# Performance work log

Hardware: AMD Instinct MI355X
Metric: run time of the kernel (lower is better)

The kernel has to match this reference:

```python
import jax, jax.numpy as jnp
import numpy as np

MARGIN = 0.5
BETA = 0.0
K = 5

def setup_inputs() -> dict:
    key = jax.random.key(0)
    k1, k2 = jax.random.split(key)
    n, d, n_classes = 4096, 512, 512
    inputs = jax.random.normal(k1, (n, d), dtype=jnp.float32)
    # L2-normalize as is standard for similarity-based DML embeddings
    inputs = inputs / jnp.linalg.norm(inputs, axis=1, keepdims=True)
    targets = jax.random.randint(k2, (n,), 0, n_classes, dtype=jnp.int64)
    return {"inputs": inputs, "targets": targets}

def reference(inputs, targets):
    n = inputs.shape[0]
    sim = inputs @ inputs.T                      # [n, n] similarity matrix
    same = targets[:, None] == targets[None, :]  # [n, n] same-class mask
    eye = jnp.eye(n, dtype=bool)
    pos_mask = same & ~eye                       # positive pairs (off-diagonal)
    neg_mask = ~same                             # negative pairs
    # margin_loss (hinge on similarity): pos -> [margin + beta - s]_+, neg -> [margin + s - beta]_+
    pos_l = jnp.maximum(MARGIN + BETA - sim, 0.0)
    neg_l = jnp.maximum(MARGIN + sim - BETA, 0.0)
    valid = pos_mask | neg_mask
    pair_loss = jnp.where(pos_mask, pos_l, neg_l)  # per-pair loss where valid
    num_of_zeros = jnp.sum(valid & (pair_loss == 0.0))
    # top-(4K) over the multiset of all valid pair losses (== topk of concat(pos_loss, neg_loss))
    masked = jnp.where(valid, pair_loss, -jnp.inf).reshape(-1)
    top_loss, _ = jax.lax.top_k(masked, 4 * K)
    loss = jnp.mean(top_loss)
    mean_pos_sim = jnp.sum(jnp.where(pos_mask, sim, 0.0)) / jnp.sum(pos_mask)
    mean_neg_sim = jnp.sum(jnp.where(neg_mask, sim, 0.0)) / jnp.sum(neg_mask)
    # NOTE: the original swaps the names: it returns mean(pos_sim) as `mean_neg_sim` and vice versa.
    return (loss, num_of_zeros, mean_pos_sim, mean_neg_sim)
```

## Files before the change

### kernel.cpp

```cpp
#include <hip/hip_runtime.h>
#include <hip/hip_fp16.h>

constexpr int N = 4096;
constexpr int D = 512;
constexpr int NT = 32;
constexpr int NBLK = NT * (NT + 1) / 2;
constexpr float SENT = -1e30f;
constexpr unsigned TCV = 8386560u;

constexpr float T0 = 0.60f;
constexpr unsigned CCAP = 320;

typedef _Float16 f16x8 __attribute__((ext_vector_type(8)));
typedef float f32x4 __attribute__((ext_vector_type(4)));

__device__ __forceinline__ void load_lds16(const _Float16* g, _Float16* l) {
  __builtin_amdgcn_global_load_lds(
      (const __attribute__((address_space(1))) void*)g,
      (__attribute__((address_space(3))) void*)l, 16, 0, 0);
}

template <int M>
__device__ __forceinline__ void wave_sel10(float (&vals)[M], float (&out)[10]) {
  int lane = threadIdx.x & 63;
  float lm = vals[0];
#pragma unroll
  for (int k = 1; k < M; k++) lm = fmaxf(lm, vals[k]);
#pragma unroll
  for (int r = 0; r < 10; r++) {
    float wmx = lm;
#pragma unroll
    for (int ofs = 1; ofs < 64; ofs <<= 1)
      wmx = fmaxf(wmx, __shfl_xor(wmx, ofs));
    out[r] = wmx;
    unsigned long long b = __ballot(lm == wmx);
    int leader = __ffsll(b) - 1;
    if (lane == leader) {
      bool found = false;
#pragma unroll
      for (int k = 0; k < M; k++) {
        bool hit = !found && (vals[k] == wmx);
        vals[k] = hit ? SENT : vals[k];
        found = found || hit;
      }
      lm = vals[0];
#pragma unroll
      for (int k = 1; k < M; k++) lm = fmaxf(lm, vals[k]);
    }
  }
}

constexpr int BMAX_IDX = 3 * NBLK;
constexpr int TOP10G_IDX = 4 * NBLK;
constexpr int XH_OFF = 32768;

__global__ void prep_kernel(const float4* __restrict__ X4,
                            ushort4* __restrict__ Xh4) {
  int gid = blockIdx.x * 256 + threadIdx.x;
  float4 v = X4[gid];
  ushort4 o;
  o.x = __half_as_ushort(__float2half_rn(v.x));
  o.y = __half_as_ushort(__float2half_rn(v.y));
  o.z = __half_as_ushort(__float2half_rn(v.z));
  o.w = __half_as_ushort(__float2half_rn(v.w));
  Xh4[gid] = o;
}

__global__ __launch_bounds__(256, 3) void gemm_stats_kernel(
    const _Float16* __restrict__ Xh, const int* __restrict__ tgt,
    float* __restrict__ slots, float* __restrict__ top10g) {
  __shared__ _Float16 As[2][128 * 32];
  __shared__ _Float16 Bs[2][128 * 32];
  __shared__ int tA[128], tB[128];
  __shared__ float redf[2][4];
  __shared__ unsigned redu[4];
  __shared__ float redm[4];
  __shared__ unsigned redc[4];
  __shared__ float cbuf[CCAP];
  __shared__ unsigned ccnt;
  __shared__ unsigned scc;

  int tid = threadIdx.x;
  if (tid == 0) ccnt = 0u;

  int id = blockIdx.x, br = 0;
  while (id >= (NT - br)) { id -= (NT - br); br++; }
  int bc = br + id;

  if (tid < 128) tA[tid] = tgt[br * 128 + tid];
  else tB[tid - 128] = tgt[bc * 128 + (tid - 128)];

  int lane = tid & 63, wave = tid >> 6;
  int wm2 = (wave >> 1) << 6;
  int wn2 = (wave & 1) << 6;
  int lrow = lane & 15;
  int q4 = lane >> 4;
  int xk = (lrow >> 1) & 3;
  int quad4 = q4 * 4;

  int srow[2], scol[2], sdst[2];
#pragma unroll
  for (int i = 0; i < 2; i++) {
    int C = i * 256 + tid;
    int row = C >> 2, p = C & 3;
    srow[i] = row;
    scol[i] = (p ^ ((row >> 1) & 3)) * 8;
    sdst[i] = (i * 4 + wave) * 512;
  }
  const _Float16* Arow = Xh + (size_t)(br * 128) * D;
  const _Float16* Brow = Xh + (size_t)(bc * 128) * D;

#pragma unroll
  for (int i = 0; i < 2; i++) {
    load_lds16(Arow + srow[i] * D + scol[i], &As[0][sdst[i]]);
    load_lds16(Brow + srow[i] * D + scol[i], &Bs[0][sdst[i]]);
  }

  f32x4 acc[4][4] = {};
#pragma unroll
  for (int t = 0; t < 16; t++) {
    int cur = t & 1;
    __syncthreads();
    if (t < 15) {
      int k0 = (t + 1) * 32;
#pragma unroll
      for (int i = 0; i < 2; i++) {
        load_lds16(Arow + srow[i] * D + k0 + scol[i], &As[cur ^ 1][sdst[i]]);
        load_lds16(Brow + srow[i] * D + k0 + scol[i], &Bs[cur ^ 1][sdst[i]]);
      }
    }
    f16x8 af[4], bf[4];
#pragma unroll
    for (int mi = 0; mi < 4; mi++)
      af[mi] = *(const f16x8*)&As[cur][(wm2 + mi * 16 + lrow) * 32 +
                                       (q4 ^ xk) * 8];
#pragma unroll
    for (int ni = 0; ni < 4; ni++)
      bf[ni] = *(const f16x8*)&Bs[cur][(wn2 + ni * 16 + lrow) * 32 +
                                       (q4 ^ xk) * 8];
#pragma unroll
    for (int mi = 0; mi < 4; mi++)
#pragma unroll
      for (int ni = 0; ni < 4; ni++)
        acc[mi][ni] = __builtin_amdgcn_mfma_f32_16x16x32_f16(
            af[mi], bf[ni], acc[mi][ni], 0, 0, 0);
  }

  int tj[4];
#pragma unroll
  for (int ni = 0; ni < 4; ni++) tj[ni] = tB[wn2 + ni * 16 + lrow];
  int ib = br * 128 + wm2 + quad4;
  int jb = bc * 128 + wn2 + lrow;

  auto forEachLoss = [&](auto&& fn) {
#pragma unroll
    for (int mi = 0; mi < 4; mi++) {
#pragma unroll
      for (int r = 0; r < 4; r++) {
        int trow = tA[wm2 + mi * 16 + quad4 + r];
        int i = ib + mi * 16 + r;
#pragma unroll
        for (int ni = 0; ni < 4; ni++) {
          float s = acc[mi][ni][r];
          int j = jb + ni * 16;
          bool valid = j > i;
          bool pos = valid && (trow == tj[ni]);
          float loss = fmaxf(0.5f + (pos ? -s : s), 0.0f);
          fn(s, loss, valid, pos);
        }
      }
    }
  };

  float lsv = 0.f, lsp = 0.f, tmax = SENT;
  unsigned cz = 0, cc = 0;
  float b0 = 0.f, b1 = 0.f, b2 = 0.f, b3 = 0.f;
  forEachLoss([&](float s, float loss, bool valid, bool pos) {
    if (valid) {
      lsv += s;
      if (loss == 0.0f) cz += 0x10000u;
      tmax = fmaxf(tmax, loss);
      if (loss >= T0) {
        if (cc == 0) b0 = loss;
        else if (cc == 1) b1 = loss;
        else if (cc == 2) b2 = loss;
        else if (cc == 3) b3 = loss;
        else {
          unsigned op = atomicAdd(&ccnt, 1u);
          if (op < CCAP) cbuf[op] = loss;
        }
        cc++;
      }
    }
    if (pos) { lsp += s; cz += 1u; }
  });

  float lmax = tmax;
#pragma unroll
  for (int o = 32; o > 0; o >>= 1) {
    lsv += __shfl_down(lsv, o);
    lsp += __shfl_down(lsp, o);
    cz += __shfl_down(cz, o);
    lmax = fmaxf(lmax, __shfl_down(lmax, o));
  }
  if (lane == 0) {
    redf[0][wave] = lsv; redf[1][wave] = lsp;
    redu[wave] = cz; redm[wave] = lmax;
  }

  unsigned cnt4 = cc < 4u ? cc : 4u;
  unsigned inc = cnt4;
#pragma unroll
  for (int o = 1; o < 64; o <<= 1) {
    unsigned tt = __shfl_up(inc, o);
    if (lane >= o) inc += tt;
  }
  unsigned base = 0;
  if (lane == 63) base = atomicAdd(&ccnt, inc);
  base = __shfl(base, 63);
  unsigned p = base + inc - cnt4;
  if (cnt4 > 0u && p < CCAP) cbuf[p] = b0;
  if (cnt4 > 1u && p + 1 < CCAP) cbuf[p + 1] = b1;
  if (cnt4 > 2u && p + 2 < CCAP) cbuf[p + 2] = b2;
  if (cnt4 > 3u && p + 3 < CCAP) cbuf[p + 3] = b3;
  __syncthreads();

  if (tid == 192) {
    float a = redf[0][0] + redf[0][1] + redf[0][2] + redf[0][3];
    float b = redf[1][0] + redf[1][1] + redf[1][2] + redf[1][3];
    unsigned c = redu[0] + redu[1] + redu[2] + redu[3];
    float bm = fmaxf(fmaxf(redm[0], redm[1]), fmaxf(redm[2], redm[3]));
    slots[blockIdx.x] = a;
    slots[NBLK + blockIdx.x] = b;
    ((unsigned*)slots)[2 * NBLK + blockIdx.x] = c;
    slots[BMAX_IDX + blockIdx.x] = bm;
  }

  unsigned cct = ccnt;
  if (cct < 10u || cct > CCAP) {
    unsigned lo = 0u, hi = 0x7f800000u;
    while (hi - lo > 1u) {
      unsigned mid = lo + (hi - lo) / 2u;
      float Tm = __uint_as_float(mid);
      unsigned c = 0;
      forEachLoss([&](float s, float loss, bool valid, bool pos) {
        (void)s; (void)pos;
        if (valid && loss >= Tm) c++;
      });
#pragma unroll
      for (int o = 32; o > 0; o >>= 1) c += __shfl_down(c, o);
      if (lane == 0) redc[wave] = c;
      __syncthreads();
      if (tid == 0) scc = redc[0] + redc[1] + redc[2] + redc[3];
      __syncthreads();
      if (scc >= 10u) lo = mid; else hi = mid;
    }
    float Tq = __uint_as_float(lo);
    if (tid == 0) ccnt = 0u;
    __syncthreads();
    forEachLoss([&](float s, float loss, bool valid, bool pos) {
      (void)s; (void)pos;
      if (valid && loss > Tq) {
        unsigned op = atomicAdd(&ccnt, 1u);
        if (op < CCAP) cbuf[op] = loss;
      }
    });
    __syncthreads();
    unsigned m = ccnt;
    if (tid < 10) cbuf[m + tid] = Tq;
    __syncthreads();
    cct = m + 10u;
  }

  if (wave == 0) {
    float m5[5];
#pragma unroll
    for (int k = 0; k < 5; k++) {
      unsigned g = lane + k * 64u;
      m5[k] = (g < cct) ? cbuf[g] : SENT;
    }
    float b10[10];
    wave_sel10<5>(m5, b10);
    if (lane == 0) {
#pragma unroll
      for (int r = 0; r < 10; r++) top10g[blockIdx.x * 10 + r] = b10[r];
    }
  }
}

__global__ __launch_bounds__(1024) void finalize_kernel(
    const float* __restrict__ slots, const float* __restrict__ top10g,
    float* __restrict__ out) {
  __shared__ float wml[160];
  __shared__ float redf[2][16];
  __shared__ unsigned redu[2][16];
  __shared__ int blist[64];
  __shared__ unsigned bcnt;
  __shared__ float gbuf[640];
  __shared__ float sT;

  int tid = threadIdx.x, lane = tid & 63, wave = tid >> 6;
  if (tid == 0) bcnt = 0u;

  float sv = 0.f, sp = 0.f;
  unsigned cv = 0, zz = 0;
  if (tid < NBLK) {
    sv = slots[tid];
    sp = slots[NBLK + tid];
    unsigned c = ((const unsigned*)slots)[2 * NBLK + tid];
    cv = c & 0xffffu;
    zz = c >> 16;
  }
  float bm = (tid < NBLK) ? slots[BMAX_IDX + tid] : SENT;
#pragma unroll
  for (int o = 32; o > 0; o >>= 1) {
    sv += __shfl_down(sv, o);
    sp += __shfl_down(sp, o);
    cv += __shfl_down(cv, o);
    zz += __shfl_down(zz, o);
  }
  if (lane == 0) {
    redf[0][wave] = sv; redf[1][wave] = sp;
    redu[0][wave] = cv; redu[1][wave] = zz;
  }

  float v1[1];
  v1[0] = bm;
  float wl[10];
  wave_sel10<1>(v1, wl);
  if (lane == 0) {
#pragma unroll
    for (int r = 0; r < 10; r++) wml[wave * 10 + r] = wl[r];
  }
  __syncthreads();
  if (wave == 0) {
    float m3[3];
#pragma unroll
    for (int k = 0; k < 3; k++) {
      int g = lane + k * 64;
      m3[k] = (g < 160) ? wml[g] : SENT;
    }
    float t10[10];
    wave_sel10<3>(m3, t10);
    if (lane == 0) sT = t10[9];
  }
  __syncthreads();
  float T = sT;

  if (tid < NBLK && bm >= T) {
    unsigned p = atomicAdd(&bcnt, 1u);
    if (p < 64u) blist[p] = tid;
  }
  __syncthreads();
  unsigned nb = bcnt;

  float f10[10];
  if (nb <= 64u) {
    unsigned ng = nb * 10u;
    if ((unsigned)tid < ng)
      gbuf[tid] = top10g[(unsigned)blist[tid / 10u] * 10u + tid % 10u];
    __syncthreads();
    if (wave == 0) {
      float mA[10];
#pragma unroll
      for (int k = 0; k < 10; k++) {
        unsigned g = lane + k * 64u;
        mA[k] = (g < ng) ? gbuf[g] : SENT;
      }
      wave_sel10<10>(mA, f10);
    }
  } else {
    float v6[6];
#pragma unroll
    for (int k = 0; k < 6; k++) {
      int g = tid + k * 1024;
      v6[k] = (g < NBLK * 10) ? top10g[g] : SENT;
    }
    float wl2[10];
    wave_sel10<6>(v6, wl2);
    if (lane == 0) {
#pragma unroll
      for (int r = 0; r < 10; r++) wml[wave * 10 + r] = wl2[r];
    }
    __syncthreads();
    if (wave == 0) {
      float m3[3];
#pragma unroll
      for (int k = 0; k < 3; k++) {
        int g = lane + k * 64;
        m3[k] = (g < 160) ? wml[g] : SENT;
      }
      wave_sel10<3>(m3, f10);
    }
  }

  if (wave == 0 && lane == 0) {
    float topsum = 0.f;
#pragma unroll
    for (int r = 0; r < 10; r++) topsum += f10[r];
    float tsv = 0.f, tsp = 0.f;
    unsigned tcv = 0, tzz = 0;
#pragma unroll
    for (int w = 0; w < 16; w++) {
      tsv += redf[0][w]; tsp += redf[1][w];
      tcv += redu[0][w]; tzz += redu[1][w];
    }
    out[0] = topsum * 0.1f;
    out[1] = (float)(2u * tzz);
    out[2] = tsp / (float)tcv;
    out[3] = (tsv - tsp) / (float)(TCV - tcv);
  }
}

extern "C" void kernel_launch(void* const* d_in, const int* in_sizes, int n_in,
                              void* d_out, int out_size, void* d_ws,
                              size_t ws_size, hipStream_t stream) {
  const float* X = (const float*)d_in[0];
  const int* tgt = (const int*)d_in[1];
  float* out = (float*)d_out;
  char* ws = (char*)d_ws;

  float* slots = (float*)ws;
  float* top10g = slots + TOP10G_IDX;
  _Float16* Xh = (_Float16*)(ws + XH_OFF);

  prep_kernel<<<(N * D / 4) / 256, 256, 0, stream>>>((const float4*)X,
                                                     (ushort4*)Xh);
  gemm_stats_kernel<<<NBLK, 256, 0, stream>>>(Xh, tgt, slots, top10g);
  finalize_kernel<<<1, 1024, 0, stream>>>(slots, top10g, out);
}
```

Before: 100.4 us.

## Load MFMA operands directly from global into registers, skip LDS staging

Replaces the LDS double-buffered tile staging (global_load_lds plus a barrier every k-step) with per-wave direct global loads of f16x8 fragments into registers, double-buffered in registers. Diagonal blocks also skip the MFMA loop for one wave whose sub-tile is entirely below the diagonal. The aim is to remove LDS traffic and the per-iteration __syncthreads. In exchange, each wave reads its own operands from global/L2 with no sharing across waves, which doubles global traffic and adds register pressure.

```diff
diff --git a/kernel.cpp b/kernel.cpp
--- a/kernel.cpp
+++ b/kernel.cpp
@@ -13,12 +13,6 @@
 
 typedef _Float16 f16x8 __attribute__((ext_vector_type(8)));
 typedef float f32x4 __attribute__((ext_vector_type(4)));
-
-__device__ __forceinline__ void load_lds16(const _Float16* g, _Float16* l) {
-  __builtin_amdgcn_global_load_lds(
-      (const __attribute__((address_space(1))) void*)g,
-      (__attribute__((address_space(3))) void*)l, 16, 0, 0);
-}
 
 template <int M>
 __device__ __forceinline__ void wave_sel10(float (&vals)[M], float (&out)[10]) {
@@ -69,8 +63,6 @@
 __global__ __launch_bounds__(256, 3) void gemm_stats_kernel(
     const _Float16* __restrict__ Xh, const int* __restrict__ tgt,
     float* __restrict__ slots, float* __restrict__ top10g) {
-  __shared__ _Float16 As[2][128 * 32];
-  __shared__ _Float16 Bs[2][128 * 32];
   __shared__ int tA[128], tB[128];
   __shared__ float redf[2][4];
   __shared__ unsigned redu[4];
@@ -95,56 +87,47 @@
   int wn2 = (wave & 1) << 6;
   int lrow = lane & 15;
   int q4 = lane >> 4;
-  int xk = (lrow >> 1) & 3;
   int quad4 = q4 * 4;
 
-  int srow[2], scol[2], sdst[2];
-#pragma unroll
-  for (int i = 0; i < 2; i++) {
-    int C = i * 256 + tid;
-    int row = C >> 2, p = C & 3;
-    srow[i] = row;
-    scol[i] = (p ^ ((row >> 1) & 3)) * 8;
-    sdst[i] = (i * 4 + wave) * 512;
-  }
-  const _Float16* Arow = Xh + (size_t)(br * 128) * D;
-  const _Float16* Brow = Xh + (size_t)(bc * 128) * D;
-
-#pragma unroll
-  for (int i = 0; i < 2; i++) {
-    load_lds16(Arow + srow[i] * D + scol[i], &As[0][sdst[i]]);
-    load_lds16(Brow + srow[i] * D + scol[i], &Bs[0][sdst[i]]);
-  }
+  const _Float16* pA[4];
+  const _Float16* pB[4];
+#pragma unroll
+  for (int mi = 0; mi < 4; mi++)
+    pA[mi] = Xh + (size_t)(br * 128 + wm2 + mi * 16 + lrow) * D + q4 * 8;
+#pragma unroll
+  for (int ni = 0; ni < 4; ni++)
+    pB[ni] = Xh + (size_t)(bc * 128 + wn2 + ni * 16 + lrow) * D + q4 * 8;
+
+  bool deadWave = (br == bc) && (wave == 2);
 
   f32x4 acc[4][4] = {};
-#pragma unroll
-  for (int t = 0; t < 16; t++) {
-    int cur = t & 1;
-    __syncthreads();
-    if (t < 15) {
-      int k0 = (t + 1) * 32;
-#pragma unroll
-      for (int i = 0; i < 2; i++) {
-        load_lds16(Arow + srow[i] * D + k0 + scol[i], &As[cur ^ 1][sdst[i]]);
-        load_lds16(Brow + srow[i] * D + k0 + scol[i], &Bs[cur ^ 1][sdst[i]]);
-      }
-    }
-    f16x8 af[4], bf[4];
-#pragma unroll
-    for (int mi = 0; mi < 4; mi++)
-      af[mi] = *(const f16x8*)&As[cur][(wm2 + mi * 16 + lrow) * 32 +
-                                       (q4 ^ xk) * 8];
-#pragma unroll
-    for (int ni = 0; ni < 4; ni++)
-      bf[ni] = *(const f16x8*)&Bs[cur][(wn2 + ni * 16 + lrow) * 32 +
-                                       (q4 ^ xk) * 8];
-#pragma unroll
-    for (int mi = 0; mi < 4; mi++)
-#pragma unroll
-      for (int ni = 0; ni < 4; ni++)
-        acc[mi][ni] = __builtin_amdgcn_mfma_f32_16x16x32_f16(
-            af[mi], bf[ni], acc[mi][ni], 0, 0, 0);
-  }
+  if (!deadWave) {
+    f16x8 af[2][4], bf[2][4];
+#pragma unroll
+    for (int mi = 0; mi < 4; mi++) af[0][mi] = *(const f16x8*)(pA[mi]);
+#pragma unroll
+    for (int ni = 0; ni < 4; ni++) bf[0][ni] = *(const f16x8*)(pB[ni]);
+#pragma unroll
+    for (int t = 0; t < 16; t++) {
+      const int cur = t & 1;
+      if (t < 15) {
+        int k1 = (t + 1) * 32;
+#pragma unroll
+        for (int mi = 0; mi < 4; mi++)
+          af[cur ^ 1][mi] = *(const f16x8*)(pA[mi] + k1);
+#pragma unroll
+        for (int ni = 0; ni < 4; ni++)
+          bf[cur ^ 1][ni] = *(const f16x8*)(pB[ni] + k1);
+      }
+#pragma unroll
+      for (int mi = 0; mi < 4; mi++)
+#pragma unroll
+        for (int ni = 0; ni < 4; ni++)
+          acc[mi][ni] = __builtin_amdgcn_mfma_f32_16x16x32_f16(
+              af[cur][mi], bf[cur][ni], acc[mi][ni], 0, 0, 0);
+    }
+  }
+  __syncthreads();
 
   int tj[4];
 #pragma unroll
```

New measurement: 129.1 us. +28.6%, slower.
